# Performance work log

Measured on AMD Instinct MI355X. Metric: run time of the kernel, lower is better.

The kernel has to match this reference:

```python
import jax, jax.numpy as jnp
import numpy as np
import math

N_HEADS = 16
ROPE_BASE = 10000.0


def _apply_rope(x_bshd, cosA, sinA):
    # x_bshd: [B,S,H,dh]; cosA/sinA: [S, dh//2]
    x1 = x_bshd[..., ::2]
    x2 = x_bshd[..., 1::2]
    c = cosA[None, :, None, :]
    s = sinA[None, :, None, :]
    # interleave rotated pairs back: [..., dh//2, 2] -> [..., dh]
    out = jnp.stack([x1 * c - x2 * s, x1 * s + x2 * c], axis=-1)
    return out.reshape(x_bshd.shape)


def setup_inputs() -> dict:
    key = jax.random.key(0)
    k1, k2, k3 = jax.random.split(key, 3)
    B, S, D = 4, 2048, 2048
    std = 1.0 / math.sqrt(D)
    x = jax.random.normal(k1, (B, S, D), dtype=jnp.float32)
    qkv_w = jax.random.normal(k2, (3 * D, D), dtype=jnp.float32) * std
    qkv_b = jnp.zeros((3 * D,), dtype=jnp.float32)
    out_w = jax.random.normal(k3, (D, D), dtype=jnp.float32) * std
    out_b = jnp.zeros((D,), dtype=jnp.float32)
    return {"x": x, "qkv_w": qkv_w, "qkv_b": qkv_b, "out_w": out_w, "out_b": out_b}


def reference(x, qkv_w, qkv_b, out_w, out_b):
    B, S, D = x.shape
    H = N_HEADS
    dh = D // H
    # fused QKV projection
    qkv = x @ qkv_w.T + qkv_b                      # [B,S,3D]
    q, k, v = jnp.split(qkv, 3, axis=-1)
    q = q.reshape(B, S, H, dh)
    k = k.reshape(B, S, H, dh)
    v = v.reshape(B, S, H, dh)
    # RoPE (interleaved pairs, base 10000)
    freqs = 1.0 / (ROPE_BASE ** (jnp.arange(0, dh, 2, dtype=jnp.float32) / dh))
    angles = jnp.arange(S, dtype=jnp.float32)[:, None] * freqs[None, :]  # [S, dh//2]
    cosA, sinA = jnp.cos(angles), jnp.sin(angles)
    q = _apply_rope(q, cosA, sinA)
    k = _apply_rope(k, cosA, sinA)
    # causal SDPA
    scale = 1.0 / math.sqrt(dh)
    scores = jnp.einsum('bshd,bthd->bhst', q, k) * scale  # [B,H,S,S]
    causal = jnp.tril(jnp.ones((S, S), dtype=bool))
    scores = jnp.where(causal[None, None], scores, jnp.finfo(scores.dtype).min)
    attn = jax.nn.softmax(scores, axis=-1)
    y = jnp.einsum('bhst,bthd->bshd', attn, v).reshape(B, S, D)
    return y @ out_w.T + out_b
```

## Files before the change

kernel.cpp:

```cpp
#include <hip/hip_runtime.h>
#include <hip/hip_bf16.h>
#include <math.h>

typedef __bf16 bf16x8 __attribute__((ext_vector_type(8)));
typedef float f32x4 __attribute__((ext_vector_type(4)));

#define GPTR(x) ((const __attribute__((address_space(1))) void*)(x))
#define LPTR(x) ((__attribute__((address_space(3))) void*)(x))

__device__ __forceinline__ void gload_lds16(const void* g, void* l) {
  __builtin_amdgcn_global_load_lds(GPTR(g), LPTR(l), 16, 0, 0);
}

__global__ __launch_bounds__(256) void cast_f32_bf16(const float* __restrict__ in,
                                                     __hip_bfloat16* __restrict__ out,
                                                     int n4) {
  int i = blockIdx.x * 256 + threadIdx.x;
  if (i >= n4) return;
  float4 v = ((const float4*)in)[i];
  __hip_bfloat16 t[4];
  t[0] = __float2bfloat16(v.x); t[1] = __float2bfloat16(v.y);
  t[2] = __float2bfloat16(v.z); t[3] = __float2bfloat16(v.w);
  ((uint2*)out)[i] = *(uint2*)t;
}

__global__ __launch_bounds__(256) void rope_tables(float* __restrict__ cosT,
                                                   float* __restrict__ sinT, int S) {
  int i = blockIdx.x * 256 + threadIdx.x;
  if (i >= S * 64) return;
  int j = i & 63, s = i >> 6;
  float freq = powf(10000.0f, -(float)(2 * j) * (1.0f / 128.0f));
  float a = (float)s * freq;
  cosT[i] = cosf(a);
  sinT[i] = sinf(a);
}

__global__ __launch_bounds__(256) void rope_apply(__hip_bfloat16* __restrict__ qkv,
                                                  const float* __restrict__ cosT,
                                                  const float* __restrict__ sinT) {
  int i = blockIdx.x * 256 + threadIdx.x;
  int jc = i & 15;
  int h = (i >> 4) & 15;
  int row = i >> 8;
  int s = row & 2047;
  float4 c4 = *(const float4*)&cosT[s * 64 + jc * 4];
  float4 s4 = *(const float4*)&sinT[s * 64 + jc * 4];
  size_t base = (size_t)row * 6144 + h * 128 + jc * 8;
#pragma unroll
  for (int half = 0; half < 2; half++) {
    __hip_bfloat16* p = qkv + base + half * 2048;
    bf16x8 v = *(bf16x8*)p;
    bf16x8 o;
    float cc[4] = {c4.x, c4.y, c4.z, c4.w};
    float ss[4] = {s4.x, s4.y, s4.z, s4.w};
#pragma unroll
    for (int u = 0; u < 4; u++) {
      float x1 = (float)v[2 * u], x2 = (float)v[2 * u + 1];
      o[2 * u]     = (__bf16)(x1 * cc[u] - x2 * ss[u]);
      o[2 * u + 1] = (__bf16)(x1 * ss[u] + x2 * cc[u]);
    }
    *(bf16x8*)p = o;
  }
}

template <int OUT_BF16>
__global__ __launch_bounds__(512, 2) void gemm256(const __hip_bfloat16* __restrict__ A,
                                                  const __hip_bfloat16* __restrict__ Bm,
                                                  const float* __restrict__ bias,
                                                  void* __restrict__ Cv,
                                                  int M, int N, int K) {
  __shared__ __align__(16) char lds[2][65536];
  const int tid = threadIdx.x, wave = tid >> 6;
  const int lane = tid & 63, l15 = lane & 15, g = lane >> 4;
  const int bm = blockIdx.y * 256, bn = blockIdx.x * 256;
  const int wr = wave >> 2, wc = wave & 3;
  f32x4 acc[8][4] = {};

  auto stage = [&](int t, int bufx, int matB, int half) {
#pragma unroll
    for (int j = 0; j < 2; j++) {
      const int rl = j * 64 + (tid >> 3);
      const int c = tid & 7;
      const int row = half * 128 + rl;
      const __hip_bfloat16* src =
          (matB ? Bm + (size_t)(bn + row) * K : A + (size_t)(bm + row) * K)
          + (size_t)t * 64 + ((c ^ (row & 7)) << 3);
      char* dst = &lds[bufx][matB * 32768 + half * 16384 + ((j * 512 + (wave << 6)) << 4)];
      gload_lds16(src, dst);
    }
  };

  const int nK = K >> 6;
  stage(0, 0, 0, 0); stage(0, 0, 0, 1); stage(0, 0, 1, 0); stage(0, 0, 1, 1);
  __syncthreads();

  int cur = 0;
  for (int t = 0; t < nK; ++t) {
    const int nb = cur ^ 1;
    const bool more = (t + 1 < nK);
#pragma unroll
    for (int ph = 0; ph < 4; ph++) {
      const int mh = ph & 1, kh = ph >> 1;
      if (ph == 0 && more) { stage(t + 1, nb, 0, 0); stage(t + 1, nb, 0, 1); }
      if (ph == 1 && more) stage(t + 1, nb, 1, 0);
      if (ph == 2 && more) stage(t + 1, nb, 1, 1);
      bf16x8 af[4], bfr[4];
#pragma unroll
      for (int i = 0; i < 4; i++) {
        const int row = wr * 128 + (mh * 4 + i) * 16 + l15;
        const int c = (kh * 4 + g) ^ (row & 7);
        af[i] = *(const bf16x8*)&lds[cur][row * 128 + c * 16];
      }
#pragma unroll
      for (int j = 0; j < 4; j++) {
        const int col = wc * 64 + j * 16 + l15;
        const int c = (kh * 4 + g) ^ (col & 7);
        bfr[j] = *(const bf16x8*)&lds[cur][32768 + col * 128 + c * 16];
      }
      __builtin_amdgcn_s_setprio(1);
#pragma unroll
      for (int i = 0; i < 4; i++)
#pragma unroll
        for (int j = 0; j < 4; j++)
          acc[mh * 4 + i][j] = __builtin_amdgcn_mfma_f32_16x16x32_bf16(
              af[i], bfr[j], acc[mh * 4 + i][j], 0, 0, 0);
      __builtin_amdgcn_s_setprio(0);
    }
    __syncthreads();
    cur = nb;
  }

  const int r0 = bm + wr * 128 + g * 4;
  const int c0 = bn + wc * 64 + l15;
#pragma unroll
  for (int fi = 0; fi < 8; fi++) {
#pragma unroll
    for (int fj = 0; fj < 4; fj++) {
      const int col = c0 + fj * 16;
      const float bv = bias[col];
#pragma unroll
      for (int r = 0; r < 4; r++) {
        const int row = r0 + fi * 16 + r;
        float v = acc[fi][fj][r] + bv;
        if (OUT_BF16)
          ((__hip_bfloat16*)Cv)[(size_t)row * N + col] = __float2bfloat16(v);
        else
          ((float*)Cv)[(size_t)row * N + col] = v;
      }
    }
  }
}

#define VTS 72
__global__ __launch_bounds__(512, 4) void flash_attn(const __hip_bfloat16* __restrict__ qkv,
                                                     __hip_bfloat16* __restrict__ y,
                                                     int S) {
  __shared__ __align__(16) char Ksm[64 * 256];
  __shared__ __align__(16) __hip_bfloat16 Vts[128 * VTS];
  const int tid = threadIdx.x, wave = tid >> 6, lane = tid & 63;
  const int l15 = lane & 15, g = lane >> 4;
  const int b = blockIdx.y >> 4, h = blockIdx.y & 15;
  const int pi = blockIdx.x;
  const size_t ldq = 6144;
  const __hip_bfloat16* Qb = qkv + (size_t)b * S * ldq + (size_t)h * 128;
  const __hip_bfloat16* Kb = Qb + 2048;
  const __hip_bfloat16* Vb = Qb + 4096;

  const int posj = ((lane >> 5) << 5) | ((((lane >> 2) & 3)) << 3) |
                   (((lane >> 4) & 1) << 2) | (lane & 3);

  for (int pass = 0; pass < 2; ++pass) {
    const int qt = pass == 0 ? (15 - pi) : pi;
    const int q0 = qt * 128;
    const int qr = q0 + wave * 16 + l15;
    const int rmin = q0 + wave * 16, rmax = rmin + 15;

    bf16x8 aq[4];
    {
      const __hip_bfloat16* qp = Qb + (size_t)qr * ldq + g * 8;
#pragma unroll
      for (int c = 0; c < 4; c++) aq[c] = *(const bf16x8*)(qp + c * 32);
    }

    float m_r = -1e30f, l_r = 0.f;
    f32x4 oacc[8] = {};
    const int nT = q0 / 64 + 2;

    int4 kreg[2], vreg[2];
#pragma unroll
    for (int i = 0; i < 2; i++) {
      int chunk = tid + i * 512, krow = chunk >> 4, kc16 = chunk & 15;
      kreg[i] = *(const int4*)((const char*)(Kb + (size_t)krow * ldq) + kc16 * 16);
      int dc = wave + 8 * i;
      vreg[i] = *(const int4*)(Vb + (size_t)lane * ldq + dc * 8);
    }

    for (int t = 0; t < nT; ++t) {
      const int kv0 = t * 64;
      __syncthreads();
#pragma unroll
      for (int i = 0; i < 2; i++) {
        int chunk = tid + i * 512, krow = chunk >> 4, kc16 = chunk & 15;
        *(int4*)&Ksm[krow * 256 + ((kc16 ^ (krow & 7)) * 16)] = kreg[i];
        int dc = wave + 8 * i;
        const __hip_bfloat16* e = (const __hip_bfloat16*)&vreg[i];
#pragma unroll
        for (int u = 0; u < 8; u++) Vts[(dc * 8 + u) * VTS + posj] = e[u];
      }
      __syncthreads();
      if (t + 1 < nT) {
        const int nkv = kv0 + 64;
#pragma unroll
        for (int i = 0; i < 2; i++) {
          int chunk = tid + i * 512, krow = chunk >> 4, kc16 = chunk & 15;
          kreg[i] = *(const int4*)((const char*)(Kb + (size_t)(nkv + krow) * ldq) + kc16 * 16);
          int dc = wave + 8 * i;
          vreg[i] = *(const int4*)(Vb + (size_t)(nkv + lane) * ldq + dc * 8);
        }
      }
      if (kv0 > rmax) continue;

      f32x4 sacc[4];
      __builtin_amdgcn_s_setprio(1);
#pragma unroll
      for (int nf = 0; nf < 4; nf++) {
        f32x4 a = {0.f, 0.f, 0.f, 0.f};
        const int n = nf * 16 + l15;
#pragma unroll
        for (int c = 0; c < 4; c++) {
          int cc = c * 4 + g;
          bf16x8 kf = *(const bf16x8*)&Ksm[n * 256 + ((cc ^ (n & 7)) * 16)];
          a = __builtin_amdgcn_mfma_f32_16x16x32_bf16(kf, aq[c], a, 0, 0, 0);
        }
        sacc[nf] = a;
      }
      __builtin_amdgcn_s_setprio(0);

      if (kv0 + 63 > rmin) {
#pragma unroll
        for (int nf = 0; nf < 4; nf++)
#pragma unroll
          for (int r = 0; r < 4; r++)
            if (kv0 + nf * 16 + g * 4 + r > qr) sacc[nf][r] = -3e38f;
      }

      const float t2e = 0.12751744f;
      float mx = sacc[0][0];
#pragma unroll
      for (int nf = 0; nf < 4; nf++)
#pragma unroll
        for (int r = 0; r < 4; r++) mx = fmaxf(mx, sacc[nf][r]);
      mx = fmaxf(mx, __shfl_xor(mx, 16, 64));
      mx = fmaxf(mx, __shfl_xor(mx, 32, 64));
      float mnew = fmaxf(m_r, mx);
      float corr = __builtin_amdgcn_exp2f((m_r - mnew) * t2e);
      m_r = mnew;
      float sum = 0.f;
#pragma unroll
      for (int nf = 0; nf < 4; nf++)
#pragma unroll
        for (int r = 0; r < 4; r++) {
          float pv = __builtin_amdgcn_exp2f((sacc[nf][r] - m_r) * t2e);
          sacc[nf][r] = pv;
          sum += pv;
        }
      sum += __shfl_xor(sum, 16, 64);
      sum += __shfl_xor(sum, 32, 64);
      l_r = l_r * corr + sum;
#pragma unroll
      for (int of = 0; of < 8; of++)
#pragma unroll
        for (int r = 0; r < 4; r++) oacc[of][r] *= corr;

      bf16x8 pa0, pa1;
#pragma unroll
      for (int r = 0; r < 4; r++) {
        pa0[r]     = (__bf16)sacc[0][r];
        pa0[r + 4] = (__bf16)sacc[1][r];
        pa1[r]     = (__bf16)sacc[2][r];
        pa1[r + 4] = (__bf16)sacc[3][r];
      }

      __builtin_amdgcn_s_setprio(1);
#pragma unroll
      for (int of = 0; of < 8; of++) {
        const int vrow = of * 16 + l15;
        bf16x8 v0 = *(const bf16x8*)&Vts[vrow * VTS + g * 8];
        bf16x8 v1 = *(const bf16x8*)&Vts[vrow * VTS + 32 + g * 8];
        oacc[of] = __builtin_amdgcn_mfma_f32_16x16x32_bf16(v0, pa0, oacc[of], 0, 0, 0);
        oacc[of] = __builtin_amdgcn_mfma_f32_16x16x32_bf16(v1, pa1, oacc[of], 0, 0, 0);
      }
      __builtin_amdgcn_s_setprio(0);
    }

    const float inv = 1.0f / l_r;
    __hip_bfloat16* yp = y + ((size_t)b * S + qr) * 2048 + h * 128;
#pragma unroll
    for (int of = 0; of < 8; of++) {
      __hip_bfloat16 o4[4];
#pragma unroll
      for (int r = 0; r < 4; r++) o4[r] = __float2bfloat16(oacc[of][r] * inv);
      *(uint2*)&yp[of * 16 + g * 4] = *(uint2*)o4;
    }
  }
}

extern "C" void kernel_launch(void* const* d_in, const int* in_sizes, int n_in,
                              void* d_out, int out_size, void* d_ws, size_t ws_size,
                              hipStream_t stream) {
  const float* x = (const float*)d_in[0];
  const float* qkv_w = (const float*)d_in[1];
  const float* qkv_b = (const float*)d_in[2];
  const float* out_w = (const float*)d_in[3];
  const float* out_b = (const float*)d_in[4];
  float* out = (float*)d_out;

  const int B = 4, S = 2048, D = 2048;
  const int M = B * S;

  char* ws = (char*)d_ws;
  __hip_bfloat16* xb   = (__hip_bfloat16*)(ws + 0);
  __hip_bfloat16* wqb  = (__hip_bfloat16*)(ws + 33554432);
  __hip_bfloat16* wob  = (__hip_bfloat16*)(ws + 58720256);
  __hip_bfloat16* qkvb = (__hip_bfloat16*)(ws + 67108864);
  __hip_bfloat16* yb   = (__hip_bfloat16*)(ws + 167772160);
  float* cosT          = (float*)(ws + 201326592);
  float* sinT          = (float*)(ws + 201850880);

  cast_f32_bf16<<<M * D / 4 / 256, 256, 0, stream>>>(x, xb, M * D / 4);
  cast_f32_bf16<<<3 * D * D / 4 / 256, 256, 0, stream>>>(qkv_w, wqb, 3 * D * D / 4);
  cast_f32_bf16<<<D * D / 4 / 256, 256, 0, stream>>>(out_w, wob, D * D / 4);
  rope_tables<<<S * 64 / 256, 256, 0, stream>>>(cosT, sinT, S);

  dim3 g1(3 * D / 256, M / 256);
  gemm256<1><<<g1, 512, 0, stream>>>(xb, wqb, qkv_b, (void*)qkvb, M, 3 * D, D);

  rope_apply<<<M, 256, 0, stream>>>(qkvb, cosT, sinT);

  dim3 g2(8, B * 16);
  flash_attn<<<g2, 512, 0, stream>>>(qkvb, yb, S);

  dim3 g3(D / 256, M / 256);
  gemm256<0><<<g3, 512, 0, stream>>>(yb, wob, out_b, (void*)out, M, D, D);
}
```

Baseline: 590.7 us.

## Restructure GEMM main loop into four-phase quadrant pipeline with fine-grained vmcnt waits

The 256x256 GEMM main loop is reorganized into four quadrant phases, each issuing one half-tile async global-to-LDS stage for the next K step. Each phase uses explicit s_waitcnt vmcnt and raw s_barrier instead of a full __syncthreads, so LDS fragment reads and MFMA work overlap the outstanding global loads. The wave-to-output mapping is changed to an interleaved row/column layout, with fragments held in registers across k-halves, and the epilogue indexing is updated to match. This adds more barriers per K step and relies on hand-counted vmcnt values for correctness.

```diff
diff --git a/kernel.cpp b/kernel.cpp
--- a/kernel.cpp
+++ b/kernel.cpp
@@ -75,6 +75,7 @@
   const int bm = blockIdx.y * 256, bn = blockIdx.x * 256;
   const int wr = wave >> 2, wc = wave & 3;
   f32x4 acc[8][4] = {};
+  bf16x8 af[4][2], bfr[4][2];
 
   auto stage = [&](int t, int bufx, int matB, int half) {
 #pragma unroll
@@ -91,56 +92,82 @@
   };
 
   const int nK = K >> 6;
-  stage(0, 0, 0, 0); stage(0, 0, 0, 1); stage(0, 0, 1, 0); stage(0, 0, 1, 1);
-  __syncthreads();
+  stage(0, 0, 0, 0); stage(0, 0, 1, 0); stage(0, 0, 1, 1); stage(0, 0, 0, 1);
+  asm volatile("s_waitcnt vmcnt(4)" ::: "memory");
+  __builtin_amdgcn_s_barrier();
+  asm volatile("" ::: "memory");
 
   int cur = 0;
   for (int t = 0; t < nK; ++t) {
     const int nb = cur ^ 1;
     const bool more = (t + 1 < nK);
-#pragma unroll
-    for (int ph = 0; ph < 4; ph++) {
-      const int mh = ph & 1, kh = ph >> 1;
-      if (ph == 0 && more) { stage(t + 1, nb, 0, 0); stage(t + 1, nb, 0, 1); }
-      if (ph == 1 && more) stage(t + 1, nb, 1, 0);
-      if (ph == 2 && more) stage(t + 1, nb, 1, 1);
-      bf16x8 af[4], bfr[4];
-#pragma unroll
-      for (int i = 0; i < 4; i++) {
-        const int row = wr * 128 + (mh * 4 + i) * 16 + l15;
-        const int c = (kh * 4 + g) ^ (row & 7);
-        af[i] = *(const bf16x8*)&lds[cur][row * 128 + c * 16];
-      }
-#pragma unroll
-      for (int j = 0; j < 4; j++) {
-        const int col = wc * 64 + j * 16 + l15;
-        const int c = (kh * 4 + g) ^ (col & 7);
-        bfr[j] = *(const bf16x8*)&lds[cur][32768 + col * 128 + c * 16];
-      }
+    const char* lc = lds[cur];
+
+    auto readA = [&](int RH) {
+#pragma unroll
+      for (int i = 0; i < 4; i++)
+#pragma unroll
+        for (int kh = 0; kh < 2; kh++) {
+          const int row = (RH * 4 + i) * 32 + wr * 16 + l15;
+          af[i][kh] = *(const bf16x8*)&lc[row * 128 + (((kh * 4 + g) ^ (row & 7)) << 4)];
+        }
+    };
+    auto readB = [&](int CH) {
+#pragma unroll
+      for (int j = 0; j < 2; j++)
+#pragma unroll
+        for (int kh = 0; kh < 2; kh++) {
+          const int col = (CH * 2 + j) * 64 + wc * 16 + l15;
+          bfr[CH * 2 + j][kh] =
+              *(const bf16x8*)&lc[32768 + col * 128 + (((kh * 4 + g) ^ (col & 7)) << 4)];
+        }
+    };
+    auto phase_sync = [&]() {
+      if (more) asm volatile("s_waitcnt vmcnt(4)" ::: "memory");
+      else      asm volatile("s_waitcnt vmcnt(0)" ::: "memory");
+      __builtin_amdgcn_s_barrier();
+      asm volatile("s_waitcnt lgkmcnt(0)" ::: "memory");
+      __builtin_amdgcn_sched_barrier(0);
+    };
+    auto mfma16 = [&](int RH, int CH) {
       __builtin_amdgcn_s_setprio(1);
 #pragma unroll
-      for (int i = 0; i < 4; i++)
-#pragma unroll
-        for (int j = 0; j < 4; j++)
-          acc[mh * 4 + i][j] = __builtin_amdgcn_mfma_f32_16x16x32_bf16(
-              af[i], bfr[j], acc[mh * 4 + i][j], 0, 0, 0);
+      for (int kh = 0; kh < 2; kh++)
+#pragma unroll
+        for (int i = 0; i < 4; i++)
+#pragma unroll
+          for (int j = 0; j < 2; j++)
+            acc[RH * 4 + i][CH * 2 + j] = __builtin_amdgcn_mfma_f32_16x16x32_bf16(
+                af[i][kh], bfr[CH * 2 + j][kh], acc[RH * 4 + i][CH * 2 + j], 0, 0, 0);
       __builtin_amdgcn_s_setprio(0);
-    }
-    __syncthreads();
+      __builtin_amdgcn_s_barrier();
+      asm volatile("" ::: "memory");
+    };
+
+    readA(0); readB(0);
+    if (more) stage(t + 1, nb, 0, 0);
+    phase_sync(); mfma16(0, 0);
+    readB(1);
+    if (more) stage(t + 1, nb, 1, 0);
+    phase_sync(); mfma16(0, 1);
+    readA(1);
+    if (more) stage(t + 1, nb, 1, 1);
+    phase_sync(); mfma16(1, 0);
+    if (more) stage(t + 1, nb, 0, 1);
+    phase_sync(); mfma16(1, 1);
+
     cur = nb;
   }
 
-  const int r0 = bm + wr * 128 + g * 4;
-  const int c0 = bn + wc * 64 + l15;
 #pragma unroll
   for (int fi = 0; fi < 8; fi++) {
 #pragma unroll
     for (int fj = 0; fj < 4; fj++) {
-      const int col = c0 + fj * 16;
+      const int col = bn + fj * 64 + wc * 16 + l15;
       const float bv = bias[col];
 #pragma unroll
       for (int r = 0; r < 4; r++) {
-        const int row = r0 + fi * 16 + r;
+        const int row = bm + fi * 32 + wr * 16 + g * 4 + r;
         float v = acc[fi][fj][r] + bv;
         if (OUT_BF16)
           ((__hip_bfloat16*)Cv)[(size_t)row * N + col] = __float2bfloat16(v);
```

Result: slower. 627.5 us (+6.2%).
